# Kernel optimization log

Hardware: AMD Instinct MI355X
Metric: run time of the kernel (lower is better)

The kernel has to match this reference:

```python
import jax, jax.numpy as jnp
import numpy as np

N_FEATURES = 16384
N_EXPERTS = 8
D_IN = 768
EXPERT_DIM = N_FEATURES // N_EXPERTS  # 2048
N_TOKENS = 16384


def setup_inputs() -> dict:
    key = jax.random.key(0)
    k_act, k_preb, k_enc, k_dec, k_rb, k_r = jax.random.split(key, 6)
    activations = jax.random.normal(k_act, (N_TOKENS, D_IN), dtype=jnp.float32)
    pre_b = jax.random.normal(k_preb, (D_IN,), dtype=jnp.float32) * 0.01
    enc = jax.random.normal(k_enc, (N_EXPERTS, D_IN, EXPERT_DIM), dtype=jnp.float32) / (2.0 ** 0.5) / (D_IN ** 0.5)
    dec = jax.random.normal(k_dec, (N_EXPERTS, EXPERT_DIM, D_IN), dtype=jnp.float32) / (EXPERT_DIM ** 0.5)
    router_b = jax.random.normal(k_rb, (D_IN,), dtype=jnp.float32) * 0.01
    router = jax.random.normal(k_r, (D_IN, N_EXPERTS), dtype=jnp.float32) / (D_IN ** 0.5)
    return {"activations": activations, "pre_b": pre_b, "enc": enc, "dec": dec,
            "router_b": router_b, "router": router}


def reference(activations, pre_b, enc, dec, router_b, router):
    # Router: softmax over experts, top-1 routing.
    logits = (activations - router_b) @ router            # [N, E]
    probs = jax.nn.softmax(logits, axis=-1)
    expert_max_prob = jnp.max(probs, axis=-1)              # [N]
    expert_idx = jnp.argmax(probs, axis=-1)                # [N] int

    n_experts = enc.shape[0]
    recons = jnp.zeros_like(activations)
    # Fixed small loop over experts; tokens are masked (zeroed) per expert so
    # each per-expert encode/decode GEMM only contributes for its routed rows.
    for e in range(n_experts):
        mask = (expert_idx == e)[:, None]                  # [N, 1]
        x_e = jnp.where(mask, activations, 0.0)            # masked gather
        latent = jax.nn.relu(x_e @ enc[e])                 # [N, expert_dim]
        recon = latent @ dec[e]                            # [N, d_in]
        recons = recons + jnp.where(mask, recon, 0.0)      # scatter-combine

    return expert_max_prob[:, None] * recons + pre_b
```

## Files before the change

kernel.cpp:

```cpp
#include <hip/hip_runtime.h>
#include <hip/hip_bf16.h>
#include <hip/hip_fp16.h>

#define N_TOKENS 16384
#define D_IN 768
#define N_EXPERTS 8
#define EXPERT_DIM 2048

#define ROUTER_BLOCKS 256
#define TOK_PER_BLOCK 64

typedef _Float16 half8 __attribute__((ext_vector_type(8)));
typedef float floatx4 __attribute__((ext_vector_type(4)));

#define BM 128
#define BN 128
#define BK 32

__device__ __forceinline__ void glds16(const _Float16* g, _Float16* l) {
    __builtin_amdgcn_global_load_lds(
        (const __attribute__((address_space(1))) unsigned int*)g,
        (__attribute__((address_space(3))) unsigned int*)l, 16, 0, 0);
}

__global__ __launch_bounds__(256) void router_kernel(const float* __restrict__ act,
    const float* __restrict__ router_b, const float* __restrict__ router,
    float* __restrict__ prob, int* __restrict__ localpos, int* __restrict__ eidx,
    int* __restrict__ hist )
{
    __shared__ int h[N_EXPERTS];
    if (threadIdx.x < N_EXPERTS) h[threadIdx.x] = 0;
    __syncthreads();

    int wave = threadIdx.x >> 6, lane = threadIdx.x & 63;
#pragma unroll 1
    for (int it = 0; it < 16; ++it) {
        int t = blockIdx.x * TOK_PER_BLOCK + wave * 16 + it;
        float acc[8];
#pragma unroll
        for (int e = 0; e < 8; ++e) acc[e] = 0.f;
        const float* arow = act + (size_t)t * D_IN;
#pragma unroll
        for (int i0 = 0; i0 < D_IN; i0 += 64) {
            int i = i0 + lane;
            float a = arow[i] - router_b[i];
            const float* r = router + i * 8;
#pragma unroll
            for (int e = 0; e < 8; ++e) acc[e] += a * r[e];
        }
#pragma unroll
        for (int s = 32; s > 0; s >>= 1) {
#pragma unroll
            for (int e = 0; e < 8; ++e) acc[e] += __shfl_down(acc[e], s, 64);
        }
        if (lane == 0) {
            float m = acc[0]; int ai = 0;
#pragma unroll
            for (int e = 1; e < 8; ++e) if (acc[e] > m) { m = acc[e]; ai = e; }
            float s = 0.f;
#pragma unroll
            for (int e = 0; e < 8; ++e) s += __expf(acc[e] - m);
            prob[t] = 1.0f / s;
            eidx[t] = ai;
            localpos[t] = atomicAdd(&h[ai], 1);
        }
    }
    __syncthreads();
    if (threadIdx.x < N_EXPERTS) hist[blockIdx.x * N_EXPERTS + threadIdx.x] = h[threadIdx.x];
}

__global__ __launch_bounds__(256) void scan_kernel(int* __restrict__ hist,
    int* __restrict__ counts, int* __restrict__ offsets)
{
    __shared__ int sh[ROUTER_BLOCKS * N_EXPERTS];
    __shared__ int tot[N_EXPERTS], off[N_EXPERTS];
    int tid = threadIdx.x;
    *(int4*)&sh[tid * 8]     = *(const int4*)&hist[tid * 8];
    *(int4*)&sh[tid * 8 + 4] = *(const int4*)&hist[tid * 8 + 4];
    __syncthreads();
    if (tid < N_EXPERTS) {
        int run = 0;
        for (int b = 0; b < ROUTER_BLOCKS; ++b) {
            int v = sh[b * 8 + tid];
            sh[b * 8 + tid] = run;
            run += v;
        }
        tot[tid] = run;
    }
    __syncthreads();
    if (tid == 0) {
        int run = 0;
        for (int e = 0; e < N_EXPERTS; ++e) {
            off[e] = run;
            offsets[e] = run;
            counts[e] = tot[e];
            run += tot[e];
        }
    }
    __syncthreads();
    int4 a = *(const int4*)&sh[tid * 8];
    int4 b = *(const int4*)&sh[tid * 8 + 4];
    a.x += off[0]; a.y += off[1]; a.z += off[2]; a.w += off[3];
    b.x += off[4]; b.y += off[5]; b.z += off[6]; b.w += off[7];
    *(int4*)&hist[tid * 8]     = a;
    *(int4*)&hist[tid * 8 + 4] = b;
}

__global__ __launch_bounds__(256) void order_kernel(const int* __restrict__ eidx,
    const int* __restrict__ localpos, const int* __restrict__ hist,
    int* __restrict__ order)
{
    int t = blockIdx.x * 256 + threadIdx.x;
    int base = hist[(t >> 6) * N_EXPERTS + eidx[t]];
    order[base + localpos[t]] = t;
}

__global__ __launch_bounds__(256) void transpose_to_half(const float* __restrict__ W,
    _Float16* __restrict__ WT, int K, int Nc)
{
    __shared__ _Float16 tile[64][72];
    size_t esz = (size_t)K * Nc;
    const float* We = W + (size_t)blockIdx.z * esz;
    _Float16* WTe = WT + (size_t)blockIdx.z * esz;
    int n0 = blockIdx.x * 64, k0 = blockIdx.y * 64;
    int tr = threadIdx.x >> 4;
    int tc = threadIdx.x & 15;
#pragma unroll
    for (int rr = 0; rr < 64; rr += 16) {
        int k = k0 + rr + tr;
        float4 v = *(const float4*)(We + (size_t)k * Nc + n0 + tc * 4);
        tile[tc * 4 + 0][rr + tr] = (_Float16)v.x;
        tile[tc * 4 + 1][rr + tr] = (_Float16)v.y;
        tile[tc * 4 + 2][rr + tr] = (_Float16)v.z;
        tile[tc * 4 + 3][rr + tr] = (_Float16)v.w;
    }
    __syncthreads();
#pragma unroll
    for (int p = 0; p < 2; ++p) {
        int id = threadIdx.x + p * 256;
        int r = id >> 3, ch = id & 7;
        half8 v = *(const half8*)&tile[r][ch * 8];
        *(half8*)(WTe + (size_t)(n0 + r) * K + k0 + ch * 8) = v;
    }
}

__global__ __launch_bounds__(256) void encode_kernel(const float* __restrict__ act,
    const _Float16* __restrict__ encT, const int* __restrict__ order,
    const int* __restrict__ counts, const int* __restrict__ offsets,
    _Float16* __restrict__ latent)
{
    int e = blockIdx.z;
    int n_e = counts[e];
    int mt = blockIdx.y;
    if (mt * BM >= n_e) return;
    int nt = blockIdx.x;
    int slot0 = offsets[e] + mt * BM;
    int mrem = n_e - mt * BM;

    __shared__ _Float16 As[BM * BK];
    __shared__ _Float16 Bs[BN * BK];
    __shared__ int s_tok[BM];

    int tid = threadIdx.x;
    if (tid < BM) s_tok[tid] = (tid < mrem) ? order[slot0 + tid] : -1;
    __syncthreads();

    const _Float16* Be = encT + (size_t)e * D_IN * EXPERT_DIM + (size_t)(nt * BN) * D_IN;

    int wave = tid >> 6, lane = tid & 63;
    int wm = wave >> 1, wn = wave & 1;

    int r0 = tid >> 2, sc = tid & 3;
    int c = (sc - (r0 >> 1)) & 3;
    int tokA0 = s_tok[r0], tokA1 = s_tok[r0 + 64];
    const float* pa0 = (tokA0 >= 0) ? act + (size_t)tokA0 * D_IN + c * 8 : nullptr;
    const float* pa1 = (tokA1 >= 0) ? act + (size_t)tokA1 * D_IN + c * 8 : nullptr;
    _Float16* wA0 = &As[r0 * BK + sc * 8];
    _Float16* wA1 = &As[(r0 + 64) * BK + sc * 8];
    const _Float16* pb0 = Be + (size_t)r0 * D_IN + c * 8;
    const _Float16* pb1 = Be + (size_t)(r0 + 64) * D_IN + c * 8;
    _Float16* lb0 = &Bs[(wave * 64) * 8];
    _Float16* lb1 = &Bs[(wave * 64 + 256) * 8];

    int frag_off = ((((lane >> 4) + ((lane & 15) >> 1)) & 3) * 8);
    int mrow = lane & 15;

    floatx4 acc[4][4];
#pragma unroll
    for (int i = 0; i < 4; ++i)
#pragma unroll
        for (int j = 0; j < 4; ++j) acc[i][j] = (floatx4){0.f, 0.f, 0.f, 0.f};

#pragma unroll 1
    for (int k0 = 0; k0 < D_IN; k0 += BK) {
        glds16(pb0 + k0, lb0);
        glds16(pb1 + k0, lb1);
        half8 h0 = {0, 0, 0, 0, 0, 0, 0, 0}, h1 = {0, 0, 0, 0, 0, 0, 0, 0};
        if (pa0) {
            float4 v0 = *(const float4*)(pa0 + k0);
            float4 v1 = *(const float4*)(pa0 + k0 + 4);
            h0[0] = (_Float16)v0.x; h0[1] = (_Float16)v0.y; h0[2] = (_Float16)v0.z; h0[3] = (_Float16)v0.w;
            h0[4] = (_Float16)v1.x; h0[5] = (_Float16)v1.y; h0[6] = (_Float16)v1.z; h0[7] = (_Float16)v1.w;
        }
        if (pa1) {
            float4 v0 = *(const float4*)(pa1 + k0);
            float4 v1 = *(const float4*)(pa1 + k0 + 4);
            h1[0] = (_Float16)v0.x; h1[1] = (_Float16)v0.y; h1[2] = (_Float16)v0.z; h1[3] = (_Float16)v0.w;
            h1[4] = (_Float16)v1.x; h1[5] = (_Float16)v1.y; h1[6] = (_Float16)v1.z; h1[7] = (_Float16)v1.w;
        }
        *(half8*)wA0 = h0;
        *(half8*)wA1 = h1;
        __syncthreads();

        half8 af[4], bf[4];
#pragma unroll
        for (int i = 0; i < 4; ++i) af[i] = *(const half8*)&As[(wm * 64 + i * 16 + mrow) * BK + frag_off];
#pragma unroll
        for (int i = 0; i < 4; ++i) bf[i] = *(const half8*)&Bs[(wn * 64 + i * 16 + mrow) * BK + frag_off];
#pragma unroll
        for (int i = 0; i < 4; ++i)
#pragma unroll
            for (int j = 0; j < 4; ++j)
                acc[i][j] = __builtin_amdgcn_mfma_f32_16x16x32_f16(af[i], bf[j], acc[i][j], 0, 0, 0);
        __syncthreads();
    }

    int crow_base = wm * 64 + (lane >> 4) * 4;
    int ccol_base = nt * BN + wn * 64 + (lane & 15);
#pragma unroll
    for (int i = 0; i < 4; ++i) {
#pragma unroll
        for (int j = 0; j < 4; ++j) {
#pragma unroll
            for (int r = 0; r < 4; ++r) {
                int row = crow_base + i * 16 + r;
                if (row < mrem) {
                    float v = acc[i][j][r];
                    v = v > 0.f ? v : 0.f;
                    latent[(size_t)(slot0 + row) * EXPERT_DIM + ccol_base + j * 16] = (_Float16)v;
                }
            }
        }
    }
}

__global__ __launch_bounds__(256) void decode_kernel(const _Float16* __restrict__ latent,
    const _Float16* __restrict__ decT, const int* __restrict__ order,
    const int* __restrict__ counts, const int* __restrict__ offsets,
    const float* __restrict__ prob, const float* __restrict__ pre_b,
    float* __restrict__ out)
{
    int e = blockIdx.z;
    int n_e = counts[e];
    int mt = blockIdx.y;
    if (mt * BM >= n_e) return;
    int nt = blockIdx.x;
    int slot0 = offsets[e] + mt * BM;
    int mrem = n_e - mt * BM;

    __shared__ _Float16 As[BM * BK];
    __shared__ _Float16 Bs[BN * BK];
    __shared__ int s_tok[BM];
    __shared__ float s_p[BM];

    int tid = threadIdx.x;
    if (tid < BM) {
        int tok = (tid < mrem) ? order[slot0 + tid] : 0;
        s_tok[tid] = tok;
        s_p[tid] = prob[tok];
    }

    const _Float16* Ae = latent + (size_t)slot0 * EXPERT_DIM;
    const _Float16* Be = decT + (size_t)e * EXPERT_DIM * D_IN + (size_t)(nt * BN) * EXPERT_DIM;

    int wave = tid >> 6, lane = tid & 63;
    int wm = wave >> 1, wn = wave & 1;

    int r0 = tid >> 2, sc = tid & 3;
    int c = (sc - (r0 >> 1)) & 3;
    const _Float16* paA0 = Ae + (size_t)r0 * EXPERT_DIM + c * 8;
    const _Float16* paA1 = Ae + (size_t)(r0 + 64) * EXPERT_DIM + c * 8;
    const _Float16* pb0 = Be + (size_t)r0 * EXPERT_DIM + c * 8;
    const _Float16* pb1 = Be + (size_t)(r0 + 64) * EXPERT_DIM + c * 8;
    _Float16* la0 = &As[(wave * 64) * 8];
    _Float16* la1 = &As[(wave * 64 + 256) * 8];
    _Float16* lb0 = &Bs[(wave * 64) * 8];
    _Float16* lb1 = &Bs[(wave * 64 + 256) * 8];

    int frag_off = ((((lane >> 4) + ((lane & 15) >> 1)) & 3) * 8);
    int mrow = lane & 15;

    floatx4 acc[4][4];
#pragma unroll
    for (int i = 0; i < 4; ++i)
#pragma unroll
        for (int j = 0; j < 4; ++j) acc[i][j] = (floatx4){0.f, 0.f, 0.f, 0.f};

#pragma unroll 1
    for (int k0 = 0; k0 < EXPERT_DIM; k0 += BK) {
        glds16(paA0 + k0, la0);
        glds16(paA1 + k0, la1);
        glds16(pb0 + k0, lb0);
        glds16(pb1 + k0, lb1);
        __syncthreads();

        half8 af[4], bf[4];
#pragma unroll
        for (int i = 0; i < 4; ++i) af[i] = *(const half8*)&As[(wm * 64 + i * 16 + mrow) * BK + frag_off];
#pragma unroll
        for (int i = 0; i < 4; ++i) bf[i] = *(const half8*)&Bs[(wn * 64 + i * 16 + mrow) * BK + frag_off];
#pragma unroll
        for (int i = 0; i < 4; ++i)
#pragma unroll
            for (int j = 0; j < 4; ++j)
                acc[i][j] = __builtin_amdgcn_mfma_f32_16x16x32_f16(af[i], bf[j], acc[i][j], 0, 0, 0);
        __syncthreads();
    }

    int crow_base = wm * 64 + (lane >> 4) * 4;
    int ccol_base = nt * BN + wn * 64 + (lane & 15);
#pragma unroll
    for (int i = 0; i < 4; ++i) {
#pragma unroll
        for (int j = 0; j < 4; ++j) {
            int col = ccol_base + j * 16;
            float pb = pre_b[col];
#pragma unroll
            for (int r = 0; r < 4; ++r) {
                int row = crow_base + i * 16 + r;
                if (row < mrem) {
                    out[(size_t)s_tok[row] * D_IN + col] = s_p[row] * acc[i][j][r] + pb;
                }
            }
        }
    }
}

extern "C" void kernel_launch(void* const* d_in, const int* in_sizes, int n_in,
                              void* d_out, int out_size, void* d_ws, size_t ws_size,
                              hipStream_t stream)
{
    const float* act      = (const float*)d_in[0];
    const float* pre_b    = (const float*)d_in[1];
    const float* enc      = (const float*)d_in[2];
    const float* dec      = (const float*)d_in[3];
    const float* router_b = (const float*)d_in[4];
    const float* router   = (const float*)d_in[5];
    float* out = (float*)d_out;

    char* w = (char*)d_ws;
    int* counts  = (int*)w;  w += 256;
    int* offsets = (int*)w;  w += 256;
    int* hist    = (int*)w;  w += ROUTER_BLOCKS * N_EXPERTS * 4;
    int* eidx    = (int*)w;  w += N_TOKENS * 4;
    int* lpos    = (int*)w;  w += N_TOKENS * 4;
    int* order   = (int*)w;  w += N_TOKENS * 4;
    float* prob  = (float*)w; w += N_TOKENS * 4;
    _Float16* encT   = (_Float16*)w; w += (size_t)N_EXPERTS * D_IN * EXPERT_DIM * 2;
    _Float16* decT   = (_Float16*)w; w += (size_t)N_EXPERTS * D_IN * EXPERT_DIM * 2;
    _Float16* latent = (_Float16*)w; w += (size_t)(N_TOKENS + BM) * EXPERT_DIM * 2;

    transpose_to_half<<<dim3(EXPERT_DIM / 64, D_IN / 64, N_EXPERTS), 256, 0, stream>>>(enc, encT, D_IN, EXPERT_DIM);
    transpose_to_half<<<dim3(D_IN / 64, EXPERT_DIM / 64, N_EXPERTS), 256, 0, stream>>>(dec, decT, EXPERT_DIM, D_IN);

    router_kernel<<<ROUTER_BLOCKS, 256, 0, stream>>>(act, router_b, router, prob, lpos, eidx, hist);
    scan_kernel<<<1, 256, 0, stream>>>(hist, counts, offsets);
    order_kernel<<<N_TOKENS / 256, 256, 0, stream>>>(eidx, lpos, hist, order);

    encode_kernel<<<dim3(EXPERT_DIM / BN, N_TOKENS / BM, N_EXPERTS), 256, 0, stream>>>(
        act, encT, order, counts, offsets, latent);
    decode_kernel<<<dim3(D_IN / BN, N_TOKENS / BM, N_EXPERTS), 256, 0, stream>>>(
        latent, decT, order, counts, offsets, prob, pre_b, out);
}
```

Baseline: 430.7 us.

## Double-buffer LDS tiles in encode/decode GEMMs and pre-convert activations to fp16

The encode and decode GEMM loops now use two LDS buffers. The next K-tile is issued with global_load_lds before computing on the current one, and explicit vmcnt waits plus raw barriers replace __syncthreads. Activations are converted to fp16 once in a separate kernel, so the encode kernel can load A through direct-to-LDS loads instead of fp32 register loads and per-tile conversion. In exchange it costs an extra kernel and workspace buffer, doubles LDS usage (which may cut occupancy), and relies on hand-coded waitcnt encodings being correct.

```diff
diff --git a/kernel.cpp b/kernel.cpp
--- a/kernel.cpp
+++ b/kernel.cpp
@@ -17,16 +17,31 @@
 #define BN 128
 #define BK 32
 
+#define WAIT_VM4 0xF74
+#define WAIT_VM0 0xF70
+
 __device__ __forceinline__ void glds16(const _Float16* g, _Float16* l) {
     __builtin_amdgcn_global_load_lds(
         (const __attribute__((address_space(1))) unsigned int*)g,
         (__attribute__((address_space(3))) unsigned int*)l, 16, 0, 0);
 }
 
+__global__ __launch_bounds__(256) void convert_act(const float* __restrict__ act,
+    _Float16* __restrict__ act_h)
+{
+    size_t i = ((size_t)blockIdx.x * 256 + threadIdx.x) * 8;
+    float4 v0 = *(const float4*)(act + i);
+    float4 v1 = *(const float4*)(act + i + 4);
+    half8 h;
+    h[0] = (_Float16)v0.x; h[1] = (_Float16)v0.y; h[2] = (_Float16)v0.z; h[3] = (_Float16)v0.w;
+    h[4] = (_Float16)v1.x; h[5] = (_Float16)v1.y; h[6] = (_Float16)v1.z; h[7] = (_Float16)v1.w;
+    *(half8*)(act_h + i) = h;
+}
+
 __global__ __launch_bounds__(256) void router_kernel(const float* __restrict__ act,
     const float* __restrict__ router_b, const float* __restrict__ router,
     float* __restrict__ prob, int* __restrict__ localpos, int* __restrict__ eidx,
-    int* __restrict__ hist )
+    int* __restrict__ hist)
 {
     __shared__ int h[N_EXPERTS];
     if (threadIdx.x < N_EXPERTS) h[threadIdx.x] = 0;
@@ -91,10 +106,7 @@
     if (tid == 0) {
         int run = 0;
         for (int e = 0; e < N_EXPERTS; ++e) {
-            off[e] = run;
-            offsets[e] = run;
-            counts[e] = tot[e];
-            run += tot[e];
+            off[e] = run; offsets[e] = run; counts[e] = tot[e]; run += tot[e];
         }
     }
     __syncthreads();
@@ -144,7 +156,7 @@
     }
 }
 
-__global__ __launch_bounds__(256) void encode_kernel(const float* __restrict__ act,
+__global__ __launch_bounds__(256) void encode_kernel(const _Float16* __restrict__ act_h,
     const _Float16* __restrict__ encT, const int* __restrict__ order,
     const int* __restrict__ counts, const int* __restrict__ offsets,
     _Float16* __restrict__ latent)
@@ -157,30 +169,25 @@
     int slot0 = offsets[e] + mt * BM;
     int mrem = n_e - mt * BM;
 
-    __shared__ _Float16 As[BM * BK];
-    __shared__ _Float16 Bs[BN * BK];
+    __shared__ _Float16 As[2][BM * BK];
+    __shared__ _Float16 Bs[2][BN * BK];
     __shared__ int s_tok[BM];
 
     int tid = threadIdx.x;
-    if (tid < BM) s_tok[tid] = (tid < mrem) ? order[slot0 + tid] : -1;
-    __syncthreads();
-
-    const _Float16* Be = encT + (size_t)e * D_IN * EXPERT_DIM + (size_t)(nt * BN) * D_IN;
+    if (tid < BM) s_tok[tid] = (tid < mrem) ? order[slot0 + tid] : 0;
+    __syncthreads();
 
     int wave = tid >> 6, lane = tid & 63;
     int wm = wave >> 1, wn = wave & 1;
 
-    int r0 = tid >> 2, sc = tid & 3;
-    int c = (sc - (r0 >> 1)) & 3;
-    int tokA0 = s_tok[r0], tokA1 = s_tok[r0 + 64];
-    const float* pa0 = (tokA0 >= 0) ? act + (size_t)tokA0 * D_IN + c * 8 : nullptr;
-    const float* pa1 = (tokA1 >= 0) ? act + (size_t)tokA1 * D_IN + c * 8 : nullptr;
-    _Float16* wA0 = &As[r0 * BK + sc * 8];
-    _Float16* wA1 = &As[(r0 + 64) * BK + sc * 8];
-    const _Float16* pb0 = Be + (size_t)r0 * D_IN + c * 8;
-    const _Float16* pb1 = Be + (size_t)(r0 + 64) * D_IN + c * 8;
-    _Float16* lb0 = &Bs[(wave * 64) * 8];
-    _Float16* lb1 = &Bs[(wave * 64 + 256) * 8];
+    int r_lo = wave * 16 + (lane >> 2);
+    int sc = lane & 3;
+    int c = (sc - (r_lo >> 1)) & 3;
+    const _Float16* Be = encT + (size_t)e * D_IN * EXPERT_DIM + (size_t)(nt * BN) * D_IN;
+    const _Float16* pa0 = act_h + (size_t)s_tok[r_lo] * D_IN + c * 8;
+    const _Float16* pa1 = act_h + (size_t)s_tok[r_lo + 64] * D_IN + c * 8;
+    const _Float16* pb0 = Be + (size_t)r_lo * D_IN + c * 8;
+    const _Float16* pb1 = Be + (size_t)(r_lo + 64) * D_IN + c * 8;
 
     int frag_off = ((((lane >> 4) + ((lane & 15) >> 1)) & 3) * 8);
     int mrow = lane & 15;
@@ -191,39 +198,40 @@
 #pragma unroll
         for (int j = 0; j < 4; ++j) acc[i][j] = (floatx4){0.f, 0.f, 0.f, 0.f};
 
+#define ENC_ISSUE(kk, buf)                                            \
+    do {                                                              \
+        int k0_ = (kk) * BK;                                          \
+        glds16(pa0 + k0_, &As[buf][(wave * 64) * 8]);                 \
+        glds16(pa1 + k0_, &As[buf][(256 + wave * 64) * 8]);           \
+        glds16(pb0 + k0_, &Bs[buf][(wave * 64) * 8]);                 \
+        glds16(pb1 + k0_, &Bs[buf][(256 + wave * 64) * 8]);           \
+    } while (0)
+
+    const int NT = D_IN / BK;
+    ENC_ISSUE(0, 0);
 #pragma unroll 1
-    for (int k0 = 0; k0 < D_IN; k0 += BK) {
-        glds16(pb0 + k0, lb0);
-        glds16(pb1 + k0, lb1);
-        half8 h0 = {0, 0, 0, 0, 0, 0, 0, 0}, h1 = {0, 0, 0, 0, 0, 0, 0, 0};
-        if (pa0) {
-            float4 v0 = *(const float4*)(pa0 + k0);
-            float4 v1 = *(const float4*)(pa0 + k0 + 4);
-            h0[0] = (_Float16)v0.x; h0[1] = (_Float16)v0.y; h0[2] = (_Float16)v0.z; h0[3] = (_Float16)v0.w;
-            h0[4] = (_Float16)v1.x; h0[5] = (_Float16)v1.y; h0[6] = (_Float16)v1.z; h0[7] = (_Float16)v1.w;
-        }
-        if (pa1) {
-            float4 v0 = *(const float4*)(pa1 + k0);
-            float4 v1 = *(const float4*)(pa1 + k0 + 4);
-            h1[0] = (_Float16)v0.x; h1[1] = (_Float16)v0.y; h1[2] = (_Float16)v0.z; h1[3] = (_Float16)v0.w;
-            h1[4] = (_Float16)v1.x; h1[5] = (_Float16)v1.y; h1[6] = (_Float16)v1.z; h1[7] = (_Float16)v1.w;
-        }
-        *(half8*)wA0 = h0;
-        *(half8*)wA1 = h1;
-        __syncthreads();
-
+    for (int k = 0; k < NT; ++k) {
+        if (k + 1 < NT) {
+            ENC_ISSUE(k + 1, (k + 1) & 1);
+            __builtin_amdgcn_s_waitcnt(WAIT_VM4);
+        } else {
+            __builtin_amdgcn_s_waitcnt(WAIT_VM0);
+        }
+        __builtin_amdgcn_s_barrier();
+        int b = k & 1;
         half8 af[4], bf[4];
 #pragma unroll
-        for (int i = 0; i < 4; ++i) af[i] = *(const half8*)&As[(wm * 64 + i * 16 + mrow) * BK + frag_off];
-#pragma unroll
-        for (int i = 0; i < 4; ++i) bf[i] = *(const half8*)&Bs[(wn * 64 + i * 16 + mrow) * BK + frag_off];
+        for (int i = 0; i < 4; ++i) af[i] = *(const half8*)&As[b][(wm * 64 + i * 16 + mrow) * BK + frag_off];
+#pragma unroll
+        for (int i = 0; i < 4; ++i) bf[i] = *(const half8*)&Bs[b][(wn * 64 + i * 16 + mrow) * BK + frag_off];
 #pragma unroll
         for (int i = 0; i < 4; ++i)
 #pragma unroll
             for (int j = 0; j < 4; ++j)
                 acc[i][j] = __builtin_amdgcn_mfma_f32_16x16x32_f16(af[i], bf[j], acc[i][j], 0, 0, 0);
-        __syncthreads();
-    }
+        __builtin_amdgcn_s_barrier();
+    }
+#undef ENC_ISSUE
 
     int crow_base = wm * 64 + (lane >> 4) * 4;
     int ccol_base = nt * BN + wn * 64 + (lane & 15);
@@ -258,8 +266,8 @@
     int slot0 = offsets[e] + mt * BM;
     int mrem = n_e - mt * BM;
 
-    __shared__ _Float16 As[BM * BK];
-    __shared__ _Float16 Bs[BN * BK];
+    __shared__ _Float16 As[2][BM * BK];
+    __shared__ _Float16 Bs[2][BN * BK];
     __shared__ int s_tok[BM];
     __shared__ float s_p[BM];
 
@@ -276,16 +284,13 @@
     int wave = tid >> 6, lane = tid & 63;
     int wm = wave >> 1, wn = wave & 1;
 
-    int r0 = tid >> 2, sc = tid & 3;
-    int c = (sc - (r0 >> 1)) & 3;
-    const _Float16* paA0 = Ae + (size_t)r0 * EXPERT_DIM + c * 8;
-    const _Float16* paA1 = Ae + (size_t)(r0 + 64) * EXPERT_DIM + c * 8;
-    const _Float16* pb0 = Be + (size_t)r0 * EXPERT_DIM + c * 8;
-    const _Float16* pb1 = Be + (size_t)(r0 + 64) * EXPERT_DIM + c * 8;
-    _Float16* la0 = &As[(wave * 64) * 8];
-    _Float16* la1 = &As[(wave * 64 + 256) * 8];
-    _Float16* lb0 = &Bs[(wave * 64) * 8];
-    _Float16* lb1 = &Bs[(wave * 64 + 256) * 8];
+    int r_lo = wave * 16 + (lane >> 2);
+    int sc = lane & 3;
+    int c = (sc - (r_lo >> 1)) & 3;
+    const _Float16* pa0 = Ae + (size_t)r_lo * EXPERT_DIM + c * 8;
+    const _Float16* pa1 = Ae + (size_t)(r_lo + 64) * EXPERT_DIM + c * 8;
+    const _Float16* pb0 = Be + (size_t)r_lo * EXPERT_DIM + c * 8;
+    const _Float16* pb1 = Be + (size_t)(r_lo + 64) * EXPERT_DIM + c * 8;
 
     int frag_off = ((((lane >> 4) + ((lane & 15) >> 1)) & 3) * 8);
     int mrow = lane & 15;
@@ -296,26 +301,40 @@
 #pragma unroll
         for (int j = 0; j < 4; ++j) acc[i][j] = (floatx4){0.f, 0.f, 0.f, 0.f};
 
+#define DEC_ISSUE(kk, buf)                                            \
+    do {                                                              \
+        int k0_ = (kk) * BK;                                          \
+        glds16(pa0 + k0_, &As[buf][(wave * 64) * 8]);                 \
+        glds16(pa1 + k0_, &As[buf][(256 + wave * 64) * 8]);           \
+        glds16(pb0 + k0_, &Bs[buf][(wave * 64) * 8]);                 \
+        glds16(pb1 + k0_, &Bs[buf][(256 + wave * 64) * 8]);           \
+    } while (0)
+
+    const int NT = EXPERT_DIM / BK;
+    DEC_ISSUE(0, 0);
 #pragma unroll 1
-    for (int k0 = 0; k0 < EXPERT_DIM; k0 += BK) {
-        glds16(paA0 + k0, la0);
-        glds16(paA1 + k0, la1);
-        glds16(pb0 + k0, lb0);
-        glds16(pb1 + k0, lb1);
-        __syncthreads();
-
+    for (int k = 0; k < NT; ++k) {
+        if (k + 1 < NT) {
+            DEC_ISSUE(k + 1, (k + 1) & 1);
+            __builtin_amdgcn_s_waitcnt(WAIT_VM4);
+        } else {
+            __builtin_amdgcn_s_waitcnt(WAIT_VM0);
+        }
+        __builtin_amdgcn_s_barrier();
+        int b = k & 1;
         half8 af[4], bf[4];
 #pragma unroll
-        for (int i = 0; i < 4; ++i) af[i] = *(const half8*)&As[(wm * 64 + i * 16 + mrow) * BK + frag_off];
-#pragma unroll
-        for (int i = 0; i < 4; ++i) bf[i] = *(const half8*)&Bs[(wn * 64 + i * 16 + mrow) * BK + frag_off];
+        for (int i = 0; i < 4; ++i) af[i] = *(const half8*)&As[b][(wm * 64 + i * 16 + mrow) * BK + frag_off];
+#pragma unroll
+        for (int i = 0; i < 4; ++i) bf[i] = *(const half8*)&Bs[b][(wn * 64 + i * 16 + mrow) * BK + frag_off];
 #pragma unroll
         for (int i = 0; i < 4; ++i)
 #pragma unroll
             for (int j = 0; j < 4; ++j)
                 acc[i][j] = __builtin_amdgcn_mfma_f32_16x16x32_f16(af[i], bf[j], acc[i][j], 0, 0, 0);
-        __syncthreads();
-    }
+        __builtin_amdgcn_s_barrier();
+    }
+#undef DEC_ISSUE
 
     int crow_base = wm * 64 + (lane >> 4) * 4;
     int ccol_base = nt * BN + wn * 64 + (lane & 15);
@@ -356,19 +375,21 @@
     int* lpos    = (int*)w;  w += N_TOKENS * 4;
     int* order   = (int*)w;  w += N_TOKENS * 4;
     float* prob  = (float*)w; w += N_TOKENS * 4;
+    _Float16* act_h  = (_Float16*)w; w += (size_t)N_TOKENS * D_IN * 2;
     _Float16* encT   = (_Float16*)w; w += (size_t)N_EXPERTS * D_IN * EXPERT_DIM * 2;
     _Float16* decT   = (_Float16*)w; w += (size_t)N_EXPERTS * D_IN * EXPERT_DIM * 2;
     _Float16* latent = (_Float16*)w; w += (size_t)(N_TOKENS + BM) * EXPERT_DIM * 2;
 
-    transpose_to_half<<<dim3(EXPERT_DIM / 64, D_IN / 64, N_EXPERTS), 256, 0, stream>>>(enc, encT, D_IN, EXPERT_DIM);
-    transpose_to_half<<<dim3(D_IN / 64, EXPERT_DIM / 64, N_EXPERTS), 256, 0, stream>>>(dec, decT, EXPERT_DIM, D_IN);
-
     router_kernel<<<ROUTER_BLOCKS, 256, 0, stream>>>(act, router_b, router, prob, lpos, eidx, hist);
     scan_kernel<<<1, 256, 0, stream>>>(hist, counts, offsets);
     order_kernel<<<N_TOKENS / 256, 256, 0, stream>>>(eidx, lpos, hist, order);
 
+    convert_act<<<N_TOKENS * D_IN / (256 * 8), 256, 0, stream>>>(act, act_h);
+    transpose_to_half<<<dim3(EXPERT_DIM / 64, D_IN / 64, N_EXPERTS), 256, 0, stream>>>(enc, encT, D_IN, EXPERT_DIM);
+    transpose_to_half<<<dim3(D_IN / 64, EXPERT_DIM / 64, N_EXPERTS), 256, 0, stream>>>(dec, decT, EXPERT_DIM, D_IN);
+
     encode_kernel<<<dim3(EXPERT_DIM / BN, N_TOKENS / BM, N_EXPERTS), 256, 0, stream>>>(
-        act, encT, order, counts, offsets, latent);
+        act_h, encT, order, counts, offsets, latent);
     decode_kernel<<<dim3(D_IN / BN, N_TOKENS / BM, N_EXPERTS), 256, 0, stream>>>(
         latent, decT, order, counts, offsets, prob, pre_b, out);
 }
```

Measured after the change: 407.9 us. 5.3% less time.
